# Performance work log

Hardware: AMD Instinct MI355X
Metric: run time of the kernel (lower is better)

The kernel has to match this reference:

```python
import jax, jax.numpy as jnp
import numpy as np

N_IMG, C_IN, H, W = 8, 8, 136, 200
N_INST = 512
CHANNELS = 8
STRIDE = 8
MASK_OUT_STRIDE = 4
# sizes_of_interest + [last*2], per __init__
SOI = jnp.asarray([64.0, 128.0, 256.0, 512.0, 1024.0, 2048.0], dtype=jnp.float32)
W_NUMS = [(C_IN + 2) * CHANNELS, CHANNELS * CHANNELS, CHANNELS]
B_NUMS = [CHANNELS, CHANNELS, 1]
N_PARAMS = sum(W_NUMS) + sum(B_NUMS)  # 169


def compute_locations(h, w, stride):
    # matches adet compute_locations: centers of stride-sized cells, (x, y)
    shifts_x = jnp.arange(w, dtype=jnp.float32) * stride + stride // 2
    shifts_y = jnp.arange(h, dtype=jnp.float32) * stride + stride // 2
    ys, xs = jnp.meshgrid(shifts_y, shifts_x, indexing='ij')
    return jnp.stack([xs.reshape(-1), ys.reshape(-1)], axis=1)  # [h*w, 2]


def bilinear_up_align_corners(x, out_h, out_w):
    # x: [n, h, w]; F.interpolate(mode='bilinear', align_corners=True)
    n, h, w = x.shape
    ys = jnp.linspace(0.0, h - 1.0, out_h)
    xs = jnp.linspace(0.0, w - 1.0, out_w)
    y0 = jnp.floor(ys).astype(jnp.int32)
    x0 = jnp.floor(xs).astype(jnp.int32)
    y1 = jnp.minimum(y0 + 1, h - 1)
    x1 = jnp.minimum(x0 + 1, w - 1)
    wy = (ys - y0.astype(jnp.float32))[None, :, None]
    wx = (xs - x0.astype(jnp.float32))[None, None, :]
    top = x[:, y0, :]
    bot = x[:, y1, :]
    row0 = top[:, :, x0] * (1.0 - wx) + top[:, :, x1] * wx
    row1 = bot[:, :, x0] * (1.0 - wx) + bot[:, :, x1] * wx
    return row0 * (1.0 - wy) + row1 * wy


def dice_coefficient(x, target):
    eps = 1e-5
    n = x.shape[0]
    x = x.reshape(n, -1)
    target = target.reshape(n, -1)
    intersection = jnp.sum(x * target, axis=1)
    union = jnp.sum(x * x, axis=1) + jnp.sum(target * target, axis=1) + eps
    return 1.0 - 2.0 * intersection / union


def setup_inputs() -> dict:
    key = jax.random.key(0)
    ks = jax.random.split(key, 6)
    mask_feats = jax.random.normal(ks[0], (N_IMG, C_IN, H, W), jnp.float32)
    mask_head_params = jax.random.normal(ks[1], (N_INST, N_PARAMS), jnp.float32) * 0.1
    instance_locations = jax.random.uniform(ks[2], (N_INST, 2), jnp.float32) * jnp.asarray(
        [W * STRIDE, H * STRIDE], dtype=jnp.float32)
    gt_masks = (jax.random.uniform(ks[3], (N_INST, 2 * H, 2 * W), jnp.float32) > 0.5).astype(jnp.float32)
    im_inds = jax.random.randint(ks[4], (N_INST,), 0, N_IMG, jnp.int32)
    fpn_levels = jax.random.randint(ks[5], (N_INST,), 0, 5, jnp.int32)
    return {
        'mask_feats': mask_feats,
        'mask_head_params': mask_head_params,
        'instance_locations': instance_locations,
        'gt_masks': gt_masks,
        'im_inds': im_inds,
        'fpn_levels': fpn_levels,
        'mask_feat_stride': 8,
    }


def reference(mask_feats, mask_head_params, instance_locations, gt_masks, im_inds, fpn_levels, mask_feat_stride):
    n_inst = mask_head_params.shape[0]
    # relative coordinates: instance center minus every grid location, / size-of-interest
    locations = compute_locations(H, W, mask_feat_stride)          # [H*W, 2]
    rel = instance_locations[:, None, :] - locations[None, :, :]   # [n, H*W, 2]
    rel = jnp.transpose(rel, (0, 2, 1)) / SOI[fpn_levels][:, None, None]
    rel = rel.reshape(n_inst, 2, H, W)
    feats = mask_feats[im_inds]                                    # gather [n, C_IN, H, W]
    x = jnp.concatenate([rel, feats], axis=1)                      # [n, C_IN+2, H, W]

    # parse_dynamic_params: split per-instance params into 1x1 conv weights/biases
    splits = np.cumsum(W_NUMS + B_NUMS)[:-1].tolist()
    p = jnp.split(mask_head_params, splits, axis=1)
    w0 = p[0].reshape(n_inst, CHANNELS, C_IN + 2)
    w1 = p[1].reshape(n_inst, CHANNELS, CHANNELS)
    w2 = p[2].reshape(n_inst, 1, CHANNELS)
    b0, b1, b2 = p[3], p[4], p[5]

    # grouped 1x1 convs (groups = n_inst) == per-instance channel GEMM
    x = jax.nn.relu(jnp.einsum('nchw,noc->nohw', x, w0) + b0[:, :, None, None])
    x = jax.nn.relu(jnp.einsum('nchw,noc->nohw', x, w1) + b1[:, :, None, None])
    logits = jnp.einsum('nchw,noc->nohw', x, w2) + b2[:, :, None, None]  # [n, 1, H, W]

    up = mask_feat_stride // MASK_OUT_STRIDE
    logits_up = bilinear_up_align_corners(logits[:, 0], H * up, W * up)
    scores = jax.nn.sigmoid(logits_up)
    loss = dice_coefficient(scores, gt_masks)                      # [n]
    return loss
```

## Files before the change

kernel.cpp:

```cpp
#include <hip/hip_runtime.h>
#include <math.h>

#define NIMG 8
#define CIN 8
#define Hh 136
#define Ww 200
#define HW (Hh * Ww)
#define OH 272
#define OW 400
#define NINST 512
#define NPAR 169
#define TROWS 34
#define NTILES 8
#define LROWS 19
#define ACHUNKS 2
#define QUADS_PER_CHUNK (HW / 4 / ACHUNKS)
#define LOG_OFF_FLOATS 16384
#define WS_NEEDED ((size_t)(LOG_OFF_FLOATS + (size_t)NINST * HW) * 4)

#define PIN(x) asm volatile("" : "+v"(x))

__global__ __launch_bounds__(256, 2) void dmh_mlp(
    const float* __restrict__ feats,
    const float* __restrict__ pars,
    const float* __restrict__ iloc,
    const int* __restrict__ iminds,
    const int* __restrict__ lvls,
    float* __restrict__ logits)
{
    const int n     = blockIdx.y;
    const int chunk = blockIdx.x;
    const int tid   = threadIdx.x;

    const float ix = iloc[2 * n + 0];
    const float iy = iloc[2 * n + 1];
    const int   im = iminds[n];
    const float invsoi = 1.0f / (float)(64 << lvls[n]);

    const float* pp = pars + n * NPAR;
    float Wf[64], w1[64], w2[8], b1[8], A0[8], Ax[8], Ay[8], b2;
#pragma unroll
    for (int o = 0; o < 8; o++) {
        const float wx0 = pp[o * 10 + 0];
        const float wy0 = pp[o * 10 + 1];
        Ax[o] = -8.0f * invsoi * wx0;
        Ay[o] = -8.0f * invsoi * wy0;
        A0[o] = pp[152 + o] + (wx0 * (ix - 4.0f) + wy0 * (iy - 4.0f)) * invsoi;
#pragma unroll
        for (int c = 0; c < 8; c++) Wf[o * 8 + c] = pp[o * 10 + 2 + c];
    }
#pragma unroll
    for (int i = 0; i < 64; i++) w1[i] = pp[80 + i];
#pragma unroll
    for (int i = 0; i < 8; i++)  w2[i] = pp[144 + i];
#pragma unroll
    for (int i = 0; i < 8; i++)  b1[i] = pp[160 + i];
    b2 = pp[168];

#pragma unroll
    for (int i = 0; i < 64; i++) PIN(Wf[i]);
#pragma unroll
    for (int i = 0; i < 64; i++) PIN(w1[i]);
#pragma unroll
    for (int i = 0; i < 8; i++) { PIN(w2[i]); PIN(b1[i]); PIN(A0[i]); PIN(Ax[i]); PIN(Ay[i]); }
    PIN(b2);

    const float* fb0 = feats + (size_t)im * (CIN * HW);
    float* lgn = logits + (size_t)n * HW;

    const int base = chunk * QUADS_PER_CHUNK;
    const int end  = base + QUADS_PER_CHUNK;
    for (int q = base + tid; q < end; q += 256) {
        const int yy = q / 50;
        const int xq = (q - yy * 50) * 4;
        const float yf = (float)yy;
        const float* fb = fb0 + yy * Ww + xq;
        float f[8][4];
#pragma unroll
        for (int c = 0; c < 8; c++) {
            const float4 t = *reinterpret_cast<const float4*>(fb + c * HW);
            f[c][0] = t.x; f[c][1] = t.y; f[c][2] = t.z; f[c][3] = t.w;
        }
        float pre[8];
#pragma unroll
        for (int o = 0; o < 8; o++) pre[o] = A0[o] + Ay[o] * yf;

        float o4[4];
#pragma unroll
        for (int p = 0; p < 4; p++) {
            const float xf = (float)(xq + p);
            float h[8];
#pragma unroll
            for (int o = 0; o < 8; o++) {
                float a = pre[o] + Ax[o] * xf;
#pragma unroll
                for (int c = 0; c < 8; c++) a += Wf[o * 8 + c] * f[c][p];
                h[o] = fmaxf(a, 0.0f);
            }
            float g[8];
#pragma unroll
            for (int o = 0; o < 8; o++) {
                float a = b1[o];
#pragma unroll
                for (int c = 0; c < 8; c++) a += w1[o * 8 + c] * h[c];
                g[o] = fmaxf(a, 0.0f);
            }
            float lg = b2;
#pragma unroll
            for (int c = 0; c < 8; c++) lg += w2[c] * g[c];
            o4[p] = lg;
        }
        *reinterpret_cast<float4*>(lgn + yy * Ww + xq) =
            make_float4(o4[0], o4[1], o4[2], o4[3]);
    }
}

__global__ __launch_bounds__(256) void dmh_dice(
    const float* __restrict__ logits,
    const float* __restrict__ gt,
    float* __restrict__ part)
{
    __shared__ float rowv[TROWS * Ww];
    __shared__ float sred[12];

    const int n    = blockIdx.y;
    const int tile = blockIdx.x;
    const int tid  = threadIdx.x;

    const float sy = 135.0f / 271.0f;
    const float sx = 199.0f / 399.0f;

    const int oy0 = tile * TROWS;
    const float* lgn = logits + (size_t)n * HW;

    for (int it = tid; it < TROWS * Ww; it += 256) {
        const int r = it / Ww;
        const int x = it - r * Ww;
        const int oy = oy0 + r;
        const float ysf = (float)oy * sy;
        const int y0 = (int)ysf;
        const float wy = ysf - (float)y0;
        const int y1 = (y0 + 1 > Hh - 1) ? (Hh - 1) : (y0 + 1);
        const float v0 = lgn[y0 * Ww + x];
        const float v1 = lgn[y1 * Ww + x];
        rowv[it] = v0 + wy * (v1 - v0);
    }
    __syncthreads();

    float aI = 0.0f, aS = 0.0f, aT = 0.0f;
    const float* gtn = gt + (size_t)n * (OH * OW) + (size_t)oy0 * OW;
    for (int g4 = tid; g4 < TROWS * (OW / 4); g4 += 256) {
        const int ry = g4 / 100;
        const int gx = (g4 - ry * 100) * 4;
        const float* rv = &rowv[ry * Ww];

        const float4 t4 = *reinterpret_cast<const float4*>(gtn + ry * OW + gx);
        const float tv[4] = { t4.x, t4.y, t4.z, t4.w };
#pragma unroll
        for (int p = 0; p < 4; p++) {
            const int ox = gx + p;
            const float xsf = (float)ox * sx;
            const int x0 = (int)xsf;
            const float wx = xsf - (float)x0;
            const int x1 = (x0 + 1 > Ww - 1) ? (Ww - 1) : (x0 + 1);
            const float a0 = rv[x0];
            const float a1 = rv[x1];
            const float v  = a0 + wx * (a1 - a0);
            const float s  = __fdividef(1.0f, 1.0f + __expf(-v));
            aI += s * tv[p];
            aS += s * s;
            aT += tv[p];
        }
    }

#pragma unroll
    for (int off = 32; off > 0; off >>= 1) {
        aI += __shfl_down(aI, off, 64);
        aS += __shfl_down(aS, off, 64);
        aT += __shfl_down(aT, off, 64);
    }
    const int wv = tid >> 6;
    if ((tid & 63) == 0) {
        sred[wv * 3 + 0] = aI;
        sred[wv * 3 + 1] = aS;
        sred[wv * 3 + 2] = aT;
    }
    __syncthreads();
    if (tid == 0) {
        float* pt = part + (size_t)(n * NTILES + tile) * 3;
        pt[0] = sred[0] + sred[3] + sred[6] + sred[9];
        pt[1] = sred[1] + sred[4] + sred[7] + sred[10];
        pt[2] = sred[2] + sred[5] + sred[8] + sred[11];
    }
}

__global__ __launch_bounds__(256) void dmh_fin2(const float* __restrict__ part,
                                                float* __restrict__ out)
{
    const int i = blockIdx.x * 256 + threadIdx.x;
    if (i < NINST) {
        float I = 0.0f, S = 0.0f, T = 0.0f;
#pragma unroll
        for (int t = 0; t < NTILES; t++) {
            const float* pt = part + (size_t)(i * NTILES + t) * 3;
            I += pt[0]; S += pt[1]; T += pt[2];
        }
        out[i] = 1.0f - 2.0f * I / (S + T + 1e-5f);
    }
}

__global__ __launch_bounds__(256) void dmh_fused(
    const float* __restrict__ feats,
    const float* __restrict__ pars,
    const float* __restrict__ iloc,
    const float* __restrict__ gt,
    const int* __restrict__ iminds,
    const int* __restrict__ lvls,
    float* __restrict__ acc)
{
    __shared__ float slog[LROWS * Ww];
    __shared__ float sred[12];
    const int n = blockIdx.y, tile = blockIdx.x, tid = threadIdx.x;
    const float* pp = pars + n * NPAR;
    float w0[80], w1[64], w2[8], b0[8], b1[8], b2;
#pragma unroll
    for (int i = 0; i < 80; i++) w0[i] = pp[i];
#pragma unroll
    for (int i = 0; i < 64; i++) w1[i] = pp[80 + i];
#pragma unroll
    for (int i = 0; i < 8; i++)  w2[i] = pp[144 + i];
#pragma unroll
    for (int i = 0; i < 8; i++)  b0[i] = pp[152 + i];
#pragma unroll
    for (int i = 0; i < 8; i++)  b1[i] = pp[160 + i];
    b2 = pp[168];
    const float ix = iloc[2 * n + 0], iy = iloc[2 * n + 1];
    const int im = iminds[n];
    const float invsoi = 1.0f / (float)(64 << lvls[n]);
    const float sy = 135.0f / 271.0f, sx = 199.0f / 399.0f;
    const int oy0 = tile * TROWS;
    const int ly0 = (int)((float)oy0 * sy);
    int lyL = (int)((float)(oy0 + TROWS - 1) * sy) + 1;
    if (lyL > Hh - 1) lyL = Hh - 1;
    const int lycnt = lyL - ly0 + 1;
    const float* fb0 = feats + (size_t)im * (CIN * HW);
    const int npix = lycnt * Ww;
    for (int i = tid; i < npix; i += 256) {
        const int yy = i / Ww;
        const int x  = i - yy * Ww;
        const int y  = ly0 + yy;
        const float r0 = (ix - (float)(x * 8 + 4)) * invsoi;
        const float r1 = (iy - (float)(y * 8 + 4)) * invsoi;
        const float* fb = fb0 + y * Ww + x;
        float f[8];
#pragma unroll
        for (int c = 0; c < 8; c++) f[c] = fb[c * HW];
        float h[8];
#pragma unroll
        for (int o = 0; o < 8; o++) {
            float a = b0[o] + w0[o * 10 + 0] * r0 + w0[o * 10 + 1] * r1;
#pragma unroll
            for (int c = 0; c < 8; c++) a += w0[o * 10 + 2 + c] * f[c];
            h[o] = fmaxf(a, 0.0f);
        }
        float g[8];
#pragma unroll
        for (int o = 0; o < 8; o++) {
            float a = b1[o];
#pragma unroll
            for (int c = 0; c < 8; c++) a += w1[o * 8 + c] * h[c];
            g[o] = fmaxf(a, 0.0f);
        }
        float lg = b2;
#pragma unroll
        for (int c = 0; c < 8; c++) lg += w2[c] * g[c];
        slog[i] = lg;
    }
    __syncthreads();
    float aI = 0.0f, aS = 0.0f, aT = 0.0f;
    const float* gtn = gt + (size_t)n * (OH * OW) + (size_t)oy0 * OW;
    for (int i = tid; i < TROWS * OW; i += 256) {
        const int ry = i / OW;
        const int ox = i - ry * OW;
        const int oy = oy0 + ry;
        const float ysf = (float)oy * sy;
        const float xsf = (float)ox * sx;
        int y0 = (int)ysf, x0 = (int)xsf;
        const float wy = ysf - (float)y0;
        const float wx = xsf - (float)x0;
        int y1 = (y0 + 1 > Hh - 1) ? (Hh - 1) : (y0 + 1);
        int x1 = (x0 + 1 > Ww - 1) ? (Ww - 1) : (x0 + 1);
        int r0i = y0 - ly0, r1i = y1 - ly0;
        r0i = r0i < 0 ? 0 : (r0i > lycnt - 1 ? lycnt - 1 : r0i);
        r1i = r1i < 0 ? 0 : (r1i > lycnt - 1 ? lycnt - 1 : r1i);
        const float v00 = slog[r0i * Ww + x0];
        const float v01 = slog[r0i * Ww + x1];
        const float v10 = slog[r1i * Ww + x0];
        const float v11 = slog[r1i * Ww + x1];
        const float top = v00 + wx * (v01 - v00);
        const float bot = v10 + wx * (v11 - v10);
        const float v   = top + wy * (bot - top);
        const float s   = __fdividef(1.0f, 1.0f + __expf(-v));
        const float t   = gtn[i];
        aI += s * t; aS += s * s; aT += t;
    }
#pragma unroll
    for (int off = 32; off > 0; off >>= 1) {
        aI += __shfl_down(aI, off, 64);
        aS += __shfl_down(aS, off, 64);
        aT += __shfl_down(aT, off, 64);
    }
    const int wv = tid >> 6;
    if ((tid & 63) == 0) {
        sred[wv * 3 + 0] = aI; sred[wv * 3 + 1] = aS; sred[wv * 3 + 2] = aT;
    }
    __syncthreads();
    if (tid == 0) {
        atomicAdd(&acc[n * 3 + 0], sred[0] + sred[3] + sred[6] + sred[9]);
        atomicAdd(&acc[n * 3 + 1], sred[1] + sred[4] + sred[7] + sred[10]);
        atomicAdd(&acc[n * 3 + 2], sred[2] + sred[5] + sred[8] + sred[11]);
    }
}

__global__ __launch_bounds__(256) void dmh_fin(const float* __restrict__ acc,
                                               float* __restrict__ out)
{
    const int i = blockIdx.x * 256 + threadIdx.x;
    if (i < NINST) {
        out[i] = 1.0f - 2.0f * acc[i * 3 + 0] / (acc[i * 3 + 1] + acc[i * 3 + 2] + 1e-5f);
    }
}

extern "C" void kernel_launch(void* const* d_in, const int* in_sizes, int n_in,
                              void* d_out, int out_size, void* d_ws, size_t ws_size,
                              hipStream_t stream) {
    const float* feats  = (const float*)d_in[0];
    const float* pars   = (const float*)d_in[1];
    const float* iloc   = (const float*)d_in[2];
    const float* gt     = (const float*)d_in[3];
    const int*   iminds = (const int*)d_in[4];
    const int*   lvls   = (const int*)d_in[5];

    if (ws_size >= WS_NEEDED) {
        float* part   = (float*)d_ws;
        float* logits = (float*)d_ws + LOG_OFF_FLOATS;
        dim3 ga(ACHUNKS, NINST);
        dmh_mlp<<<ga, 256, 0, stream>>>(feats, pars, iloc, iminds, lvls, logits);
        dim3 gb(NTILES, NINST);
        dmh_dice<<<gb, 256, 0, stream>>>(logits, gt, part);
        dmh_fin2<<<(NINST + 255) / 256, 256, 0, stream>>>(part, (float*)d_out);
    } else {
        float* acc = (float*)d_ws;
        hipMemsetAsync(acc, 0, NINST * 3 * sizeof(float), stream);
        dim3 grid(NTILES, NINST);
        dmh_fused<<<grid, 256, 0, stream>>>(feats, pars, iloc, gt, iminds, lvls, acc);
        dmh_fin<<<(NINST + 255) / 256, 256, 0, stream>>>(acc, (float*)d_out);
    }
}
```

Measured before the change: 427.2 us.

## Prefetch next feature quad in MLP loop and halve dice tile height

The MLP kernel now software-pipelines its feature loads, fetching the next iteration's eight float4 channel vectors while computing the current quad. This is meant to hide global memory latency. The extra live registers are accommodated by relaxing launch bounds from 2 to 1 block per CU. The dice kernel tiles are halved to 17 output rows with 16 tiles per instance, which gives more blocks and a smaller shared buffer; the partial-sum workspace offset is doubled and the fallback fused path keeps its old 34-row tiling hardcoded.

```diff
diff --git a/kernel.cpp b/kernel.cpp
--- a/kernel.cpp
+++ b/kernel.cpp
@@ -10,17 +10,17 @@
 #define OW 400
 #define NINST 512
 #define NPAR 169
-#define TROWS 34
-#define NTILES 8
+#define TROWS 17
+#define NTILES 16
 #define LROWS 19
 #define ACHUNKS 2
 #define QUADS_PER_CHUNK (HW / 4 / ACHUNKS)
-#define LOG_OFF_FLOATS 16384
+#define LOG_OFF_FLOATS 32768
 #define WS_NEEDED ((size_t)(LOG_OFF_FLOATS + (size_t)NINST * HW) * 4)
 
 #define PIN(x) asm volatile("" : "+v"(x))
 
-__global__ __launch_bounds__(256, 2) void dmh_mlp(
+__global__ __launch_bounds__(256, 1) void dmh_mlp(
     const float* __restrict__ feats,
     const float* __restrict__ pars,
     const float* __restrict__ iloc,
@@ -70,17 +70,33 @@
 
     const int base = chunk * QUADS_PER_CHUNK;
     const int end  = base + QUADS_PER_CHUNK;
-    for (int q = base + tid; q < end; q += 256) {
+
+    int q = base + tid;
+    float4 cf[8];
+    if (q < end) {
+        const int yy = q / 50;
+        const int xq = (q - yy * 50) * 4;
+        const float* fb = fb0 + yy * Ww + xq;
+#pragma unroll
+        for (int c = 0; c < 8; c++)
+            cf[c] = *reinterpret_cast<const float4*>(fb + c * HW);
+    }
+
+    for (; q < end; q += 256) {
+        const int qn = q + 256;
+        float4 nf[8];
+        if (qn < end) {
+            const int yyn = qn / 50;
+            const int xqn = (qn - yyn * 50) * 4;
+            const float* fbn = fb0 + yyn * Ww + xqn;
+#pragma unroll
+            for (int c = 0; c < 8; c++)
+                nf[c] = *reinterpret_cast<const float4*>(fbn + c * HW);
+        }
+
         const int yy = q / 50;
         const int xq = (q - yy * 50) * 4;
         const float yf = (float)yy;
-        const float* fb = fb0 + yy * Ww + xq;
-        float f[8][4];
-#pragma unroll
-        for (int c = 0; c < 8; c++) {
-            const float4 t = *reinterpret_cast<const float4*>(fb + c * HW);
-            f[c][0] = t.x; f[c][1] = t.y; f[c][2] = t.z; f[c][3] = t.w;
-        }
         float pre[8];
 #pragma unroll
         for (int o = 0; o < 8; o++) pre[o] = A0[o] + Ay[o] * yf;
@@ -89,12 +105,17 @@
 #pragma unroll
         for (int p = 0; p < 4; p++) {
             const float xf = (float)(xq + p);
+            const float fp[8] = {
+                ((const float*)&cf[0])[p], ((const float*)&cf[1])[p],
+                ((const float*)&cf[2])[p], ((const float*)&cf[3])[p],
+                ((const float*)&cf[4])[p], ((const float*)&cf[5])[p],
+                ((const float*)&cf[6])[p], ((const float*)&cf[7])[p] };
             float h[8];
 #pragma unroll
             for (int o = 0; o < 8; o++) {
                 float a = pre[o] + Ax[o] * xf;
 #pragma unroll
-                for (int c = 0; c < 8; c++) a += Wf[o * 8 + c] * f[c][p];
+                for (int c = 0; c < 8; c++) a += Wf[o * 8 + c] * fp[c];
                 h[o] = fmaxf(a, 0.0f);
             }
             float g[8];
@@ -112,6 +133,9 @@
         }
         *reinterpret_cast<float4*>(lgn + yy * Ww + xq) =
             make_float4(o4[0], o4[1], o4[2], o4[3]);
+
+#pragma unroll
+        for (int c = 0; c < 8; c++) cf[c] = nf[c];
     }
 }
 
@@ -238,9 +262,9 @@
     const int im = iminds[n];
     const float invsoi = 1.0f / (float)(64 << lvls[n]);
     const float sy = 135.0f / 271.0f, sx = 199.0f / 399.0f;
-    const int oy0 = tile * TROWS;
+    const int oy0 = tile * 34;
     const int ly0 = (int)((float)oy0 * sy);
-    int lyL = (int)((float)(oy0 + TROWS - 1) * sy) + 1;
+    int lyL = (int)((float)(oy0 + 34 - 1) * sy) + 1;
     if (lyL > Hh - 1) lyL = Hh - 1;
     const int lycnt = lyL - ly0 + 1;
     const float* fb0 = feats + (size_t)im * (CIN * HW);
@@ -279,7 +303,7 @@
     __syncthreads();
     float aI = 0.0f, aS = 0.0f, aT = 0.0f;
     const float* gtn = gt + (size_t)n * (OH * OW) + (size_t)oy0 * OW;
-    for (int i = tid; i < TROWS * OW; i += 256) {
+    for (int i = tid; i < 34 * OW; i += 256) {
         const int ry = i / OW;
         const int ox = i - ry * OW;
         const int oy = oy0 + ry;
@@ -352,7 +376,7 @@
     } else {
         float* acc = (float*)d_ws;
         hipMemsetAsync(acc, 0, NINST * 3 * sizeof(float), stream);
-        dim3 grid(NTILES, NINST);
+        dim3 grid(8, NINST);
         dmh_fused<<<grid, 256, 0, stream>>>(feats, pars, iloc, gt, iminds, lvls, acc);
         dmh_fin<<<(NINST + 255) / 256, 256, 0, stream>>>(acc, (float*)d_out);
     }
```

New measurement: 456.8 us. +6.9%, slower.

## Split MLP layer-0 channels across half-blocks and exchange activations via LDS

Applied to the files above, without the earlier changes.

The per-pixel MLP kernel now has each half of the block compute four of the eight first-layer output channels for a quad of pixels. It writes them to a double-buffered shared-memory tile, and after a barrier each thread finishes layers 1 and 2 for one pixel. This halves the first-layer weight registers per thread to raise occupancy. The grid also grows from 2 to 8 chunks per instance, at the cost of a block barrier per iteration and extra LDS traffic. The fused-path constants are inlined, which does not change behaviour.

```diff
diff --git a/kernel.cpp b/kernel.cpp
--- a/kernel.cpp
+++ b/kernel.cpp
@@ -13,8 +13,12 @@
 #define TROWS 34
 #define NTILES 8
 #define LROWS 19
-#define ACHUNKS 2
-#define QUADS_PER_CHUNK (HW / 4 / ACHUNKS)
+#define ACHUNKS 8
+#define CHUNK_PX (HW / ACHUNKS)
+#define IT_PX 512
+#define AITERS ((CHUNK_PX + IT_PX - 1) / IT_PX)
+#define QSTRIDE 36
+#define LDSH (128 * QSTRIDE)
 #define LOG_OFF_FLOATS 16384
 #define WS_NEEDED ((size_t)(LOG_OFF_FLOATS + (size_t)NINST * HW) * 4)
 
@@ -28,9 +32,13 @@
     const int* __restrict__ lvls,
     float* __restrict__ logits)
 {
+    __shared__ float hbuf[2 * LDSH];
+
     const int n     = blockIdx.y;
     const int chunk = blockIdx.x;
     const int tid   = threadIdx.x;
+    const int qi    = tid & 127;
+    const int half  = tid >> 7;
 
     const float ix = iloc[2 * n + 0];
     const float iy = iloc[2 * n + 1];
@@ -38,17 +46,20 @@
     const float invsoi = 1.0f / (float)(64 << lvls[n]);
 
     const float* pp = pars + n * NPAR;
-    float Wf[64], w1[64], w2[8], b1[8], A0[8], Ax[8], Ay[8], b2;
-#pragma unroll
-    for (int o = 0; o < 8; o++) {
+
+    float Wf[32], A0[4], Ax[4], Ay[4];
+#pragma unroll
+    for (int j = 0; j < 4; j++) {
+        const int o = half * 4 + j;
         const float wx0 = pp[o * 10 + 0];
         const float wy0 = pp[o * 10 + 1];
-        Ax[o] = -8.0f * invsoi * wx0;
-        Ay[o] = -8.0f * invsoi * wy0;
-        A0[o] = pp[152 + o] + (wx0 * (ix - 4.0f) + wy0 * (iy - 4.0f)) * invsoi;
-#pragma unroll
-        for (int c = 0; c < 8; c++) Wf[o * 8 + c] = pp[o * 10 + 2 + c];
-    }
+        Ax[j] = -8.0f * invsoi * wx0;
+        Ay[j] = -8.0f * invsoi * wy0;
+        A0[j] = pp[152 + o] + (wx0 * (ix - 4.0f) + wy0 * (iy - 4.0f)) * invsoi;
+#pragma unroll
+        for (int c = 0; c < 8; c++) Wf[j * 8 + c] = pp[o * 10 + 2 + c];
+    }
+    float w1[64], w2[8], b1[8], b2;
 #pragma unroll
     for (int i = 0; i < 64; i++) w1[i] = pp[80 + i];
 #pragma unroll
@@ -58,60 +69,76 @@
     b2 = pp[168];
 
 #pragma unroll
-    for (int i = 0; i < 64; i++) PIN(Wf[i]);
+    for (int i = 0; i < 32; i++) PIN(Wf[i]);
+#pragma unroll
+    for (int i = 0; i < 4; i++) { PIN(A0[i]); PIN(Ax[i]); PIN(Ay[i]); }
 #pragma unroll
     for (int i = 0; i < 64; i++) PIN(w1[i]);
 #pragma unroll
-    for (int i = 0; i < 8; i++) { PIN(w2[i]); PIN(b1[i]); PIN(A0[i]); PIN(Ax[i]); PIN(Ay[i]); }
+    for (int i = 0; i < 8; i++) { PIN(w2[i]); PIN(b1[i]); }
     PIN(b2);
 
     const float* fb0 = feats + (size_t)im * (CIN * HW);
     float* lgn = logits + (size_t)n * HW;
 
-    const int base = chunk * QUADS_PER_CHUNK;
-    const int end  = base + QUADS_PER_CHUNK;
-    for (int q = base + tid; q < end; q += 256) {
-        const int yy = q / 50;
-        const int xq = (q - yy * 50) * 4;
-        const float yf = (float)yy;
-        const float* fb = fb0 + yy * Ww + xq;
-        float f[8][4];
-#pragma unroll
-        for (int c = 0; c < 8; c++) {
-            const float4 t = *reinterpret_cast<const float4*>(fb + c * HW);
-            f[c][0] = t.x; f[c][1] = t.y; f[c][2] = t.z; f[c][3] = t.w;
-        }
-        float pre[8];
-#pragma unroll
-        for (int o = 0; o < 8; o++) pre[o] = A0[o] + Ay[o] * yf;
-
-        float o4[4];
-#pragma unroll
-        for (int p = 0; p < 4; p++) {
-            const float xf = (float)(xq + p);
-            float h[8];
-#pragma unroll
-            for (int o = 0; o < 8; o++) {
-                float a = pre[o] + Ax[o] * xf;
-#pragma unroll
-                for (int c = 0; c < 8; c++) a += Wf[o * 8 + c] * f[c][p];
-                h[o] = fmaxf(a, 0.0f);
+    const int cbase = chunk * CHUNK_PX;
+    int buf = 0;
+
+    for (int it = 0; it < AITERS; it++) {
+        const int base = cbase + it * IT_PX;
+        const int cnt  = (CHUNK_PX - it * IT_PX < IT_PX) ? (CHUNK_PX - it * IT_PX) : IT_PX;
+
+        if (qi * 4 < cnt) {
+            const int gpx = base + qi * 4;
+            const int y   = gpx / Ww;
+            const int x   = gpx - y * Ww;
+            const float yf = (float)y;
+            const float* fb = fb0 + gpx;
+            float f[8][4];
+#pragma unroll
+            for (int c = 0; c < 8; c++) {
+                const float4 t = *reinterpret_cast<const float4*>(fb + c * HW);
+                f[c][0] = t.x; f[c][1] = t.y; f[c][2] = t.z; f[c][3] = t.w;
             }
-            float g[8];
-#pragma unroll
-            for (int o = 0; o < 8; o++) {
-                float a = b1[o];
-#pragma unroll
-                for (int c = 0; c < 8; c++) a += w1[o * 8 + c] * h[c];
-                g[o] = fmaxf(a, 0.0f);
+            float* hb = &hbuf[buf * LDSH + qi * QSTRIDE + half * 4];
+#pragma unroll
+            for (int p = 0; p < 4; p++) {
+                const float xf = (float)(x + p);
+                float4 hv;
+                float* hvp = (float*)&hv;
+#pragma unroll
+                for (int j = 0; j < 4; j++) {
+                    float a = A0[j] + Ax[j] * xf + Ay[j] * yf;
+#pragma unroll
+                    for (int c = 0; c < 8; c++) a += Wf[j * 8 + c] * f[c][p];
+                    hvp[j] = fmaxf(a, 0.0f);
+                }
+                *reinterpret_cast<float4*>(hb + p * 8) = hv;
             }
-            float lg = b2;
-#pragma unroll
-            for (int c = 0; c < 8; c++) lg += w2[c] * g[c];
-            o4[p] = lg;
-        }
-        *reinterpret_cast<float4*>(lgn + yy * Ww + xq) =
-            make_float4(o4[0], o4[1], o4[2], o4[3]);
+        }
+        __syncthreads();
+
+#pragma unroll
+        for (int s = 0; s < 2; s++) {
+            const int pl = tid + s * 256;
+            if (pl < cnt) {
+                const int q = pl >> 2, p = pl & 3;
+                const float* hb = &hbuf[buf * LDSH + q * QSTRIDE + p * 8];
+                const float4 h0 = *reinterpret_cast<const float4*>(hb);
+                const float4 h1 = *reinterpret_cast<const float4*>(hb + 4);
+                const float hv[8] = { h0.x, h0.y, h0.z, h0.w, h1.x, h1.y, h1.z, h1.w };
+                float lg = b2;
+#pragma unroll
+                for (int o = 0; o < 8; o++) {
+                    float a = b1[o];
+#pragma unroll
+                    for (int c = 0; c < 8; c++) a += w1[o * 8 + c] * hv[c];
+                    lg += w2[o] * fmaxf(a, 0.0f);
+                }
+                lgn[base + pl] = lg;
+            }
+        }
+        buf ^= 1;
     }
 }
 
@@ -238,9 +265,9 @@
     const int im = iminds[n];
     const float invsoi = 1.0f / (float)(64 << lvls[n]);
     const float sy = 135.0f / 271.0f, sx = 199.0f / 399.0f;
-    const int oy0 = tile * TROWS;
+    const int oy0 = tile * 34;
     const int ly0 = (int)((float)oy0 * sy);
-    int lyL = (int)((float)(oy0 + TROWS - 1) * sy) + 1;
+    int lyL = (int)((float)(oy0 + 34 - 1) * sy) + 1;
     if (lyL > Hh - 1) lyL = Hh - 1;
     const int lycnt = lyL - ly0 + 1;
     const float* fb0 = feats + (size_t)im * (CIN * HW);
@@ -279,7 +306,7 @@
     __syncthreads();
     float aI = 0.0f, aS = 0.0f, aT = 0.0f;
     const float* gtn = gt + (size_t)n * (OH * OW) + (size_t)oy0 * OW;
-    for (int i = tid; i < TROWS * OW; i += 256) {
+    for (int i = tid; i < 34 * OW; i += 256) {
         const int ry = i / OW;
         const int ox = i - ry * OW;
         const int oy = oy0 + ry;
@@ -352,7 +379,7 @@
     } else {
         float* acc = (float*)d_ws;
         hipMemsetAsync(acc, 0, NINST * 3 * sizeof(float), stream);
-        dim3 grid(NTILES, NINST);
+        dim3 grid(8, NINST);
         dmh_fused<<<grid, 256, 0, stream>>>(feats, pars, iloc, gt, iminds, lvls, acc);
         dmh_fin<<<(NINST + 255) / 256, 256, 0, stream>>>(acc, (float*)d_out);
     }
```

Measured after the change: 433.1 us. Within noise of the previous version (+1.4%).
